# Kernel optimization log

Measured on AMD Instinct MI355X. Metric: run time of the kernel, lower is better.

## Reference

```python
import jax, jax.numpy as jnp
import numpy as np

B, S, D, O, E, K = 4, 1024, 512, 512, 8, 2


def setup_inputs() -> dict:
    key = jax.random.key(0)
    ks = jax.random.split(key, 9)
    sd = 1.0 / np.sqrt(D)
    so = 1.0 / np.sqrt(O)
    return {
        "x": jax.random.normal(ks[0], (B, S, D), dtype=jnp.float32),
        "gate_w": jax.random.uniform(ks[1], (D, E), minval=-sd, maxval=sd, dtype=jnp.float32),
        "gate_b": jax.random.uniform(ks[2], (E,), minval=-sd, maxval=sd, dtype=jnp.float32),
        "w1": jax.random.uniform(ks[3], (E, D, O), minval=-sd, maxval=sd, dtype=jnp.float32),
        "b1": jax.random.uniform(ks[4], (E, O), minval=-sd, maxval=sd, dtype=jnp.float32),
        "w2": jax.random.uniform(ks[5], (E, O, O), minval=-so, maxval=so, dtype=jnp.float32),
        "b2": jax.random.uniform(ks[6], (E, O), minval=-so, maxval=so, dtype=jnp.float32),
        "w3": jax.random.uniform(ks[7], (E, O, O), minval=-so, maxval=so, dtype=jnp.float32),
        "b3": jax.random.uniform(ks[8], (E, O), minval=-so, maxval=so, dtype=jnp.float32),
    }


def reference(x, gate_w, gate_b, w1, b1, w2, b2, w3, b3):
    # Gating: softmax over experts, then top-k expert selection per token.
    logits = jnp.einsum('bsd,de->bse', x, gate_w) + gate_b
    probs = jax.nn.softmax(logits, axis=-1)                 # [B,S,E]
    _, top_idx = jax.lax.top_k(probs, K)                    # [B,S,K]

    n = B * S
    xt = x.reshape(n, D)
    idx_f = top_idx.reshape(n, K)
    # Faithful quirk of the original: the combine weight for slot j is
    # gateProbabilities[b, s, j] (indexing by the SLOT index, not the
    # selected expert id), because nonzero() yields the top-k slot column.
    slot_w = probs.reshape(n, E)[:, :K]                     # [n,K]

    # Dense per-expert 3-layer MLP (grouped GEMM baseline).
    h = jax.nn.relu(jnp.einsum('nd,edh->enh', xt, w1) + b1[:, None, :])
    h = jax.nn.relu(jnp.einsum('enh,eho->eno', h, w2) + b2[:, None, :])
    y = jax.nn.relu(jnp.einsum('enh,eho->eno', h, w3) + b3[:, None, :])  # [E,n,O]

    # combine[n,e] = sum_j 1[top_idx[n,j]==e] * slot_w[n,j]
    combine = jnp.einsum('nke,nk->ne', jax.nn.one_hot(idx_f, E, dtype=xt.dtype), slot_w)
    out = jnp.einsum('ne,eno->no', combine, y)
    return out.reshape(B, S, O)
```

## Files before the change

kernel.cpp:

```cpp
#include <hip/hip_runtime.h>
#include <hip/hip_bf16.h>
#include <float.h>


#define NTOK   4096
#define DIM    512
#define NEXP   8
#define MATSZ  (DIM * DIM)

typedef _Float16 half8 __attribute__((ext_vector_type(8)));
typedef float    f32x4 __attribute__((ext_vector_type(4)));

#define META_OFF   0u
#define TOPE_OFF   1024u
#define TOPW_OFF   33792u
#define ETOK_OFF   66560u
#define EW_OFF     197632u
#define XH_OFF     328704u
#define WT_OFF     4523008u

__device__ __forceinline__ int swz(int row) {
    return ((row & 7) << 3) ^ ((row & 8) << 1);
}

__global__ __launch_bounds__(256)
void gate_kernel(const float* __restrict__ x, const float* __restrict__ gw,
                 const float* __restrict__ gb,
                 int* __restrict__ top_e, float* __restrict__ top_w,
                 _Float16* __restrict__ xh, float* __restrict__ out)
{
    int tid = threadIdx.x;
    int n = blockIdx.x * 4 + (tid >> 6);
    int lane = tid & 63;

    float4 z = {0.f, 0.f, 0.f, 0.f};
    float* op = out + (size_t)n * DIM + lane * 8;
    *(float4*)op = z;
    *(float4*)(op + 4) = z;

    const float* xr = x + (size_t)n * DIM + lane * 8;
    float4 v0 = *(const float4*)xr;
    float4 v1 = *(const float4*)(xr + 4);
    float xv[8] = {v0.x, v0.y, v0.z, v0.w, v1.x, v1.y, v1.z, v1.w};

    half8 h = { (_Float16)xv[0], (_Float16)xv[1], (_Float16)xv[2], (_Float16)xv[3],
                (_Float16)xv[4], (_Float16)xv[5], (_Float16)xv[6], (_Float16)xv[7] };
    *(half8*)(xh + (size_t)n * DIM + lane * 8) = h;

    float p[NEXP];
#pragma unroll
    for (int e = 0; e < NEXP; e++) p[e] = 0.f;
    const float* g = gw + (size_t)lane * 64;
#pragma unroll
    for (int j = 0; j < 8; j++)
#pragma unroll
        for (int e = 0; e < NEXP; e++) p[e] += xv[j] * g[j * 8 + e];
#pragma unroll
    for (int e = 0; e < NEXP; e++) {
        float v = p[e];
        for (int off = 32; off; off >>= 1) v += __shfl_xor(v, off, 64);
        p[e] = v;
    }
    if (lane == 0) {
        float l[NEXP];
#pragma unroll
        for (int e = 0; e < NEXP; e++) l[e] = p[e] + gb[e];
        float m = l[0];
#pragma unroll
        for (int e = 1; e < NEXP; e++) m = fmaxf(m, l[e]);
        float ex[NEXP], s = 0.f;
#pragma unroll
        for (int e = 0; e < NEXP; e++) { ex[e] = expf(l[e] - m); s += ex[e]; }
        int e0 = 0; float m0 = l[0];
#pragma unroll
        for (int e = 1; e < NEXP; e++) if (l[e] > m0) { m0 = l[e]; e0 = e; }
        int e1 = -1; float m1 = -FLT_MAX;
#pragma unroll
        for (int e = 0; e < NEXP; e++) if (e != e0 && l[e] > m1) { m1 = l[e]; e1 = e; }
        float inv = 1.f / s;
        top_e[2 * n + 0] = e0;
        top_e[2 * n + 1] = e1;
        top_w[2 * n + 0] = ex[0] * inv;
        top_w[2 * n + 1] = ex[1] * inv;
    }
}

__global__ __launch_bounds__(256)
void scatter_kernel(const int* __restrict__ top_e, const float* __restrict__ top_w,
                    int* __restrict__ meta, int* __restrict__ entry_tok,
                    float* __restrict__ entry_w)
{
    int n = blockIdx.x * 256 + threadIdx.x;
    int lane = threadIdx.x & 63;
#pragma unroll
    for (int j = 0; j < 2; j++) {
        int e = top_e[2 * n + j];
        float ww = top_w[2 * n + j];
        int pos = 0;
        for (int ex = 0; ex < NEXP; ex++) {
            unsigned long long m = __ballot(e == ex);
            if (e == ex) {
                int leader = __ffsll(m) - 1;
                int base = 0;
                if (lane == leader) base = atomicAdd(&meta[8 + ex], __popcll(m));
                base = __shfl(base, leader, 64);
                pos = (ex << 12) + base + __popcll(m & ((1ull << lane) - 1ull));
            }
        }
        entry_tok[pos] = n;
        entry_w[pos] = ww;
    }
}

__global__ __launch_bounds__(256)
void pack_w(const float* __restrict__ W1, const float* __restrict__ W2,
            const float* __restrict__ W3, _Float16* __restrict__ Wt)
{
    __shared__ float s[32 * 513];
    int bid = blockIdx.x;
    int mat = bid >> 4, kc = bid & 15;
    const float* src = ((mat < 8) ? W1 + (size_t)mat * MATSZ
                      : (mat < 16) ? W2 + (size_t)(mat - 8) * MATSZ
                                   : W3 + (size_t)(mat - 16) * MATSZ)
                     + (size_t)kc * 32 * DIM;
    int tid = threadIdx.x;
#pragma unroll
    for (int i = 0; i < 16; i++) {
        int idx = i * 1024 + tid * 4;
        int k = idx >> 9, c = idx & 511;
        float4 v = *(const float4*)(src + idx);
        float* d = &s[k * 513 + c];
        d[0] = v.x; d[1] = v.y; d[2] = v.z; d[3] = v.w;
    }
    __syncthreads();
    int w = tid >> 6, lane = tid & 63, l15 = lane & 15, l4 = lane >> 4;
#pragma unroll
    for (int i = 0; i < 8; i++) {
        int c16 = w * 8 + i;
        int col = c16 * 16 + l15;
        half8 h;
#pragma unroll
        for (int j = 0; j < 8; j++)
            h[j] = (_Float16)s[(l4 * 8 + j) * 513 + col];
        *(half8*)(Wt + (size_t)mat * MATSZ + (size_t)(kc * 32 + c16) * 512 + lane * 8) = h;
    }
}

__global__ __launch_bounds__(512, 2)
void fused_mlp(const _Float16* __restrict__ xh, const _Float16* __restrict__ wt,
               const float* __restrict__ b1, const float* __restrict__ b2,
               const float* __restrict__ b3, float* __restrict__ out,
               const int* __restrict__ meta, const int* __restrict__ entry_tok,
               const float* __restrict__ entry_w)
{
    __shared__ _Float16 hbuf[64 * DIM];
    __shared__ int   rtok[64];
    __shared__ float rw[64];

    int bid = blockIdx.x;
    int e = bid & 7;
    int j = bid >> 3;
    int cnt = meta[8 + e];
    if (j >= ((cnt + 63) >> 6)) return;
    int row0 = (e << 12) + (j << 6);

    int tid = threadIdx.x;
    int w = tid >> 6, l = tid & 63;
    int l15 = l & 15, l4 = l >> 4;
    int colb = w * 64 + l15;

    if (tid < 64) {
        int t = entry_tok[row0 + tid];
        rtok[tid] = t;
        rw[tid]   = entry_w[row0 + tid];
    }
    __syncthreads();

    {
        int row = tid >> 3;
        int c0 = (tid & 7) * 64;
        int tk = rtok[row]; if (tk < 0) tk = 0;
        const _Float16* src = xh + (size_t)tk * DIM + c0;
        int f = swz(row);
        _Float16* dst = hbuf + row * DIM;
#pragma unroll
        for (int q = 0; q < 8; q++) {
            half8 v = *(const half8*)(src + q * 8);
            *(half8*)(dst + ((c0 + q * 8) ^ f)) = v;
        }
    }
    __syncthreads();

    f32x4 acc[4][4];

    auto run_layer = [&](const _Float16* __restrict__ Wp) {
#pragma unroll
        for (int rg = 0; rg < 4; rg++)
#pragma unroll
            for (int cg = 0; cg < 4; cg++) acc[rg][cg] = (f32x4){0.f, 0.f, 0.f, 0.f};
        const _Float16* wb = Wp + (size_t)(w * 4) * 512 + (size_t)l * 8;
        half8 b[2][4];
#pragma unroll
        for (int cg = 0; cg < 4; cg++)
            b[0][cg] = *(const half8*)(wb + (size_t)cg * 512);
#pragma unroll
        for (int kc = 0; kc < 16; kc++) {
            const int cur = kc & 1, nxt = cur ^ 1;
            const int kn = (kc + 1) & 15;
#pragma unroll
            for (int cg = 0; cg < 4; cg++)
                b[nxt][cg] = *(const half8*)(wb + (size_t)(kn * 32 + cg) * 512);
            int koff = kc * 32 + l4 * 8;
            half8 af[4];
#pragma unroll
            for (int rg = 0; rg < 4; rg++) {
                int row = rg * 16 + l15;
                af[rg] = *(const half8*)(hbuf + row * DIM + (koff ^ swz(row)));
            }
#pragma unroll
            for (int rg = 0; rg < 4; rg++)
#pragma unroll
                for (int cg = 0; cg < 4; cg++)
                    acc[rg][cg] = __builtin_amdgcn_mfma_f32_16x16x32_f16(af[rg], b[cur][cg], acc[rg][cg], 0, 0, 0);
        }
    };

    auto writeback = [&](const float* __restrict__ Bias) {
        float bs[4];
#pragma unroll
        for (int cg = 0; cg < 4; cg++) bs[cg] = Bias[e * DIM + colb + cg * 16];
        __syncthreads();
#pragma unroll
        for (int rg = 0; rg < 4; rg++)
#pragma unroll
            for (int r = 0; r < 4; r++) {
                int row = rg * 16 + l4 * 4 + r;
                int f = swz(row);
                _Float16* dst = hbuf + row * DIM;
#pragma unroll
                for (int cg = 0; cg < 4; cg++)
                    dst[(colb + cg * 16) ^ f] = (_Float16)fmaxf(acc[rg][cg][r] + bs[cg], 0.f);
            }
        __syncthreads();
    };

    run_layer(wt + (size_t)e * MATSZ);        writeback(b1);
    run_layer(wt + (size_t)(8 + e) * MATSZ);  writeback(b2);
    run_layer(wt + (size_t)(16 + e) * MATSZ);

    float bs[4];
#pragma unroll
    for (int cg = 0; cg < 4; cg++) bs[cg] = b3[e * DIM + colb + cg * 16];
#pragma unroll
    for (int rg = 0; rg < 4; rg++)
#pragma unroll
        for (int r = 0; r < 4; r++) {
            int row = rg * 16 + l4 * 4 + r;
            int tok = rtok[row];
            if (tok >= 0) {
                float ww = rw[row];
                float* op = out + (size_t)tok * DIM + colb;
#pragma unroll
                for (int cg = 0; cg < 4; cg++) {
                    float v = fmaxf(acc[rg][cg][r] + bs[cg], 0.f);
                    atomicAdd(op + cg * 16, ww * v);
                }
            }
        }
}

extern "C" void kernel_launch(void* const* d_in, const int* in_sizes, int n_in,
                              void* d_out, int out_size, void* d_ws, size_t ws_size,
                              hipStream_t stream)
{
    const float* x      = (const float*)d_in[0];
    const float* gate_w = (const float*)d_in[1];
    const float* gate_b = (const float*)d_in[2];
    const float* w1     = (const float*)d_in[3];
    const float* b1     = (const float*)d_in[4];
    const float* w2     = (const float*)d_in[5];
    const float* b2     = (const float*)d_in[6];
    const float* w3     = (const float*)d_in[7];
    const float* b3     = (const float*)d_in[8];
    float* out = (float*)d_out;

    char* ws = (char*)d_ws;
    int*      meta      = (int*)(ws + META_OFF);
    int*      top_e     = (int*)(ws + TOPE_OFF);
    float*    top_w     = (float*)(ws + TOPW_OFF);
    int*      entry_tok = (int*)(ws + ETOK_OFF);
    float*    entry_w   = (float*)(ws + EW_OFF);
    _Float16* xh        = (_Float16*)(ws + XH_OFF);
    _Float16* wt        = (_Float16*)(ws + WT_OFF);

    hipMemsetAsync(meta, 0, 256, stream);

    gate_kernel<<<NTOK / 4, 256, 0, stream>>>(x, gate_w, gate_b, top_e, top_w, xh, out);
    scatter_kernel<<<NTOK / 256, 256, 0, stream>>>(top_e, top_w, meta, entry_tok, entry_w);
    pack_w<<<24 * 16, 256, 0, stream>>>(w1, w2, w3, wt);

    fused_mlp<<<NEXP * 64, 512, 0, stream>>>(xh, wt, b1, b2, b3, out,
                                             meta, entry_tok, entry_w);
}
```

Before: 161.1 us.

## Warp-specialize fused MLP into weight-loading producers and MFMA consumer waves

New measurement: 174.5 us. 1.08x slower.

```diff
diff --git a/kernel.cpp b/kernel.cpp
--- a/kernel.cpp
+++ b/kernel.cpp
@@ -146,7 +146,7 @@
     }
 }
 
-__global__ __launch_bounds__(512, 2)
+__global__ __launch_bounds__(512, 1)
 void fused_mlp(const _Float16* __restrict__ xh, const _Float16* __restrict__ wt,
                const float* __restrict__ b1, const float* __restrict__ b2,
                const float* __restrict__ b3, float* __restrict__ out,
@@ -154,8 +154,11 @@
                const float* __restrict__ entry_w)
 {
     __shared__ _Float16 hbuf[64 * DIM];
+    __shared__ _Float16 ring[4][2][4096];
     __shared__ int   rtok[64];
     __shared__ float rw[64];
+    __shared__ int   pflag[4];
+    __shared__ int   cflag[4];
 
     int bid = blockIdx.x;
     int e = bid & 7;
@@ -167,19 +170,18 @@
     int tid = threadIdx.x;
     int w = tid >> 6, l = tid & 63;
     int l15 = l & 15, l4 = l >> 4;
-    int colb = w * 64 + l15;
 
     if (tid < 64) {
-        int t = entry_tok[row0 + tid];
-        rtok[tid] = t;
+        rtok[tid] = entry_tok[row0 + tid];
         rw[tid]   = entry_w[row0 + tid];
     }
-    __syncthreads();
+    if (tid < 4) { pflag[tid] = 0; cflag[tid] = 0; }
 
     {
         int row = tid >> 3;
         int c0 = (tid & 7) * 64;
         int tk = rtok[row]; if (tk < 0) tk = 0;
+        tk = entry_tok[row0 + row]; if (tk < 0) tk = 0;
         const _Float16* src = xh + (size_t)tk * DIM + c0;
         int f = swz(row);
         _Float16* dst = hbuf + row * DIM;
@@ -191,82 +193,110 @@
     }
     __syncthreads();
 
-    f32x4 acc[4][4];
-
-    auto run_layer = [&](const _Float16* __restrict__ Wp) {
-#pragma unroll
-        for (int rg = 0; rg < 4; rg++)
-#pragma unroll
-            for (int cg = 0; cg < 4; cg++) acc[rg][cg] = (f32x4){0.f, 0.f, 0.f, 0.f};
-        const _Float16* wb = Wp + (size_t)(w * 4) * 512 + (size_t)l * 8;
-        half8 b[2][4];
-#pragma unroll
-        for (int cg = 0; cg < 4; cg++)
-            b[0][cg] = *(const half8*)(wb + (size_t)cg * 512);
-#pragma unroll
-        for (int kc = 0; kc < 16; kc++) {
-            const int cur = kc & 1, nxt = cur ^ 1;
-            const int kn = (kc + 1) & 15;
-#pragma unroll
-            for (int cg = 0; cg < 4; cg++)
-                b[nxt][cg] = *(const half8*)(wb + (size_t)(kn * 32 + cg) * 512);
-            int koff = kc * 32 + l4 * 8;
-            half8 af[4];
-#pragma unroll
-            for (int rg = 0; rg < 4; rg++) {
-                int row = rg * 16 + l15;
-                af[rg] = *(const half8*)(hbuf + row * DIM + (koff ^ swz(row)));
-            }
+    const bool is_prod = (w >= 4);
+    const int  pr = w & 3;
+
+    if (is_prod) {
+        for (int layer = 0; layer < 3; layer++) {
+            const _Float16* Wp = wt + (size_t)(layer * 8 + e) * MATSZ;
+            const _Float16* wb = Wp + (size_t)(pr * 8) * 512 + (size_t)l * 8;
+            half8 r[2][8];
+#pragma unroll
+            for (int cg = 0; cg < 8; cg++)
+                r[0][cg] = *(const half8*)(wb + (size_t)cg * 512);
+            for (int kc = 0; kc < 16; kc++) {
+                int gs = layer * 16 + kc;
+                if (kc + 1 < 16) {
+#pragma unroll
+                    for (int cg = 0; cg < 8; cg++)
+                        r[(kc + 1) & 1][cg] =
+                            *(const half8*)(wb + (size_t)((kc + 1) * 32 + cg) * 512);
+                }
+                while (*(volatile int*)&cflag[pr] < gs - 1) __builtin_amdgcn_s_sleep(1);
+                __threadfence_block();
+                _Float16* dst = &ring[pr][gs & 1][0];
+#pragma unroll
+                for (int cg = 0; cg < 8; cg++)
+                    *(half8*)(dst + cg * 512 + l * 8) = r[kc & 1][cg];
+                __threadfence_block();
+                if (l == 0) *(volatile int*)&pflag[pr] = gs + 1;
+            }
+            if (layer < 2) {
+                __syncthreads();
+                __syncthreads();
+            }
+        }
+    } else {
+        f32x4 acc[4][8];
+        int colb = pr * 128 + l15;
+        const float* Bs[3] = {b1, b2, b3};
+        for (int layer = 0; layer < 3; layer++) {
 #pragma unroll
             for (int rg = 0; rg < 4; rg++)
 #pragma unroll
-                for (int cg = 0; cg < 4; cg++)
-                    acc[rg][cg] = __builtin_amdgcn_mfma_f32_16x16x32_f16(af[rg], b[cur][cg], acc[rg][cg], 0, 0, 0);
+                for (int cg = 0; cg < 8; cg++) acc[rg][cg] = (f32x4){0.f, 0.f, 0.f, 0.f};
+            for (int kc = 0; kc < 16; kc++) {
+                int gs = layer * 16 + kc;
+                while (*(volatile int*)&pflag[pr] < gs + 1) __builtin_amdgcn_s_sleep(1);
+                __threadfence_block();
+                const _Float16* slot = &ring[pr][gs & 1][0];
+                int koff = kc * 32 + l4 * 8;
+                half8 af[4], bf[8];
+#pragma unroll
+                for (int rg = 0; rg < 4; rg++) {
+                    int row = rg * 16 + l15;
+                    af[rg] = *(const half8*)(hbuf + row * DIM + (koff ^ swz(row)));
+                }
+#pragma unroll
+                for (int cg = 0; cg < 8; cg++)
+                    bf[cg] = *(const half8*)(slot + cg * 512 + l * 8);
+#pragma unroll
+                for (int rg = 0; rg < 4; rg++)
+#pragma unroll
+                    for (int cg = 0; cg < 8; cg++)
+                        acc[rg][cg] = __builtin_amdgcn_mfma_f32_16x16x32_f16(af[rg], bf[cg], acc[rg][cg], 0, 0, 0);
+                __threadfence_block();
+                if (l == 0) *(volatile int*)&cflag[pr] = gs + 1;
+            }
+            if (layer < 2) {
+                float bs[8];
+#pragma unroll
+                for (int cg = 0; cg < 8; cg++) bs[cg] = Bs[layer][e * DIM + colb + cg * 16];
+                __syncthreads();
+#pragma unroll
+                for (int rg = 0; rg < 4; rg++)
+#pragma unroll
+                    for (int r = 0; r < 4; r++) {
+                        int row = rg * 16 + l4 * 4 + r;
+                        int f = swz(row);
+                        _Float16* dst = hbuf + row * DIM;
+#pragma unroll
+                        for (int cg = 0; cg < 8; cg++)
+                            dst[(colb + cg * 16) ^ f] = (_Float16)fmaxf(acc[rg][cg][r] + bs[cg], 0.f);
+                    }
+                __syncthreads();
+            }
         }
-    };
-
-    auto writeback = [&](const float* __restrict__ Bias) {
-        float bs[4];
-#pragma unroll
-        for (int cg = 0; cg < 4; cg++) bs[cg] = Bias[e * DIM + colb + cg * 16];
-        __syncthreads();
+        float bs[8];
+#pragma unroll
+        for (int cg = 0; cg < 8; cg++) bs[cg] = b3[e * DIM + colb + cg * 16];
 #pragma unroll
         for (int rg = 0; rg < 4; rg++)
 #pragma unroll
             for (int r = 0; r < 4; r++) {
                 int row = rg * 16 + l4 * 4 + r;
-                int f = swz(row);
-                _Float16* dst = hbuf + row * DIM;
-#pragma unroll
-                for (int cg = 0; cg < 4; cg++)
-                    dst[(colb + cg * 16) ^ f] = (_Float16)fmaxf(acc[rg][cg][r] + bs[cg], 0.f);
-            }
-        __syncthreads();
-    };
-
-    run_layer(wt + (size_t)e * MATSZ);        writeback(b1);
-    run_layer(wt + (size_t)(8 + e) * MATSZ);  writeback(b2);
-    run_layer(wt + (size_t)(16 + e) * MATSZ);
-
-    float bs[4];
-#pragma unroll
-    for (int cg = 0; cg < 4; cg++) bs[cg] = b3[e * DIM + colb + cg * 16];
-#pragma unroll
-    for (int rg = 0; rg < 4; rg++)
-#pragma unroll
-        for (int r = 0; r < 4; r++) {
-            int row = rg * 16 + l4 * 4 + r;
-            int tok = rtok[row];
-            if (tok >= 0) {
-                float ww = rw[row];
-                float* op = out + (size_t)tok * DIM + colb;
-#pragma unroll
-                for (int cg = 0; cg < 4; cg++) {
-                    float v = fmaxf(acc[rg][cg][r] + bs[cg], 0.f);
-                    atomicAdd(op + cg * 16, ww * v);
+                int tok = rtok[row];
+                if (tok >= 0) {
+                    float ww = rw[row];
+                    float* op = out + (size_t)tok * DIM + colb;
+#pragma unroll
+                    for (int cg = 0; cg < 8; cg++) {
+                        float v = fmaxf(acc[rg][cg][r] + bs[cg], 0.f);
+                        atomicAdd(op + cg * 16, ww * v);
+                    }
                 }
             }
-        }
+    }
 }
 
 extern "C" void kernel_launch(void* const* d_in, const int* in_sizes, int n_in,
```
